# Kernel tuning notes

Measured on AMD Instinct MI355X. Metric: run time of the kernel, lower is better.

The kernel has to match this reference:

```python
import jax, jax.numpy as jnp
import numpy as np


def setup_inputs() -> dict:
    key = jax.random.key(0)
    k1, k2 = jax.random.split(key)
    x = jax.random.normal(k1, (8, 4096, 256), dtype=jnp.float32)
    embed = jax.random.normal(k2, (1, 8192, 256), dtype=jnp.float32)
    return {"x": x, "embed": embed}


def reference(x, embed):
    # EuclideanCodebook.forward, eval mode, sample_codebook_temp=0.
    # x: [b, n, d]  (ndim < 4 -> a leading codebook dim h=1 is added)
    # embed: [h, c, d]
    xf = x.astype(jnp.float32)[None]              # [h, b, n, d]
    h, b, n, d = xf.shape
    flatten = xf.reshape(h, b * n, d)             # [h, N, d]

    # dist = -cdist(flatten, embed, p=2)
    x2 = jnp.sum(flatten * flatten, axis=-1, keepdims=True)   # [h, N, 1]
    e2 = jnp.sum(embed * embed, axis=-1)                      # [h, c]
    xe = jnp.einsum('hnd,hcd->hnc', flatten, embed)           # [h, N, c]
    d2 = jnp.maximum(x2 + e2[:, None, :] - 2.0 * xe, 0.0)
    dist = -jnp.sqrt(d2)                                      # [h, N, c]

    # gumbel_sample with temperature == 0  ->  argmax
    embed_ind = jnp.argmax(dist, axis=-1)                     # [h, N]
    embed_ind = embed_ind.reshape(h, b, n)                    # [h, b, n]

    # batched_embedding: gather codes per codebook
    quantize = jax.vmap(lambda e, i: e[i])(embed, embed_ind)  # [h, b, n, d]

    # needs_codebook_dim -> squeeze leading h
    return quantize[0], embed_ind[0]
```

## Files before the change

### kernel.cpp

```cpp
#include <hip/hip_runtime.h>
#include <math.h>

#define D       256
#define NROWS   32768
#define CODES   8192
#define QOFF    8388608

#define BM      128
#define BN      128
#define BK      64
#define NSPL    4
#define SPLC    (CODES / NSPL)
#define NCHUNK  (SPLC / BN)
#define NBLK    1024
#define LQ      4096

#define MARG_COEF 0.016f
#define MARG_ABS  0.10f

#define OFF_AH    0ull
#define OFF_X2    16777216ull
#define OFF_NX    16908288ull
#define OFF_E2    17039360ull
#define OFF_RM    17072128ull
#define OFF_PK    17203200ull
#define OFF_MISC  17465344ull
#define OFF_BCNT  17465600ull
#define OFF_CAND  17469696ull
#define WS_NEED3  38441216ull

typedef __attribute__((ext_vector_type(8)))  short bf16x8;
typedef __attribute__((ext_vector_type(16))) float f32x16;

__device__ __forceinline__ int SWK(int b) { return b ^ (((b >> 7) & 7) << 4); }

__device__ __forceinline__ void gload16(const void* g, void* l) {
  __builtin_amdgcn_global_load_lds(
      (const __attribute__((address_space(1))) unsigned int*)g,
      (__attribute__((address_space(3))) unsigned int*)l, 16, 0, 0);
}

__device__ __forceinline__ unsigned short bf16rn(float x) {
  unsigned u = __float_as_uint(x);
  return (unsigned short)((u + 0x7fffu + ((u >> 16) & 1u)) >> 16);
}

__device__ __forceinline__ unsigned encf(float f) {
  unsigned b = __float_as_uint(f);
  return (b >> 31) ? ~b : (b | 0x80000000u);
}
__device__ __forceinline__ float decf(unsigned u) {
  return __uint_as_float((u >> 31) ? (u ^ 0x80000000u) : ~u);
}

__global__ __launch_bounds__(256) void init_kernel(unsigned* __restrict__ misc,
                                                   unsigned* __restrict__ rowMinU,
                                                   unsigned long long* __restrict__ pKey) {
  int i = blockIdx.x * 256 + threadIdx.x;
  if (i < 16) misc[i] = 0u;
  rowMinU[i] = 0xFFFFFFFFu;
  pKey[i] = ~0ull;
}

__global__ __launch_bounds__(256) void prep_kernel(const float* __restrict__ x,
                                                   const float* __restrict__ embed,
                                                   unsigned short* __restrict__ A_h,
                                                   unsigned short* __restrict__ E_h,
                                                   float* __restrict__ x2,
                                                   float* __restrict__ nx,
                                                   float* __restrict__ e2,
                                                   unsigned* __restrict__ misc) {
  int wid  = threadIdx.x >> 6;
  int lane = threadIdx.x & 63;
  int rid  = blockIdx.x * 4 + wid;
  const float* src;
  unsigned short* dst;
  if (rid < NROWS) { src = x + (size_t)rid * D;               dst = A_h + (size_t)rid * D; }
  else             { src = embed + (size_t)(rid - NROWS) * D; dst = E_h + (size_t)(rid - NROWS) * D; }
  float4 v = *(const float4*)(src + lane * 4);
  ushort4 hv = make_ushort4(bf16rn(v.x), bf16rn(v.y), bf16rn(v.z), bf16rn(v.w));
  *(ushort4*)(dst + lane * 4) = hv;
  float p = v.x * v.x + v.y * v.y + v.z * v.z + v.w * v.w;
  #pragma unroll
  for (int off = 32; off > 0; off >>= 1) p += __shfl_down(p, off);
  if (lane == 0) {
    float n = sqrtf(p);
    if (rid < NROWS) { x2[rid] = p; nx[rid] = n; }
    else { e2[rid - NROWS] = p; atomicMax(&misc[2], __float_as_uint(n)); }
  }
}

template<int MODE>
__global__ __launch_bounds__(256, 2) void gemm_pass(
    const unsigned short* __restrict__ A_h,
    const unsigned short* __restrict__ E_h,
    const float* __restrict__ e2g,
    const float* __restrict__ nxg,
    const unsigned* __restrict__ miscR,
    unsigned* __restrict__ rowMinU,
    unsigned* __restrict__ cand,
    unsigned* __restrict__ blkCnt,
    unsigned* __restrict__ ovCnt,
    unsigned Q, unsigned OVCAP) {
  __shared__ __align__(16) char As[16384];
  __shared__ __align__(16) char Bs[16384];
  __shared__ unsigned lbuf[MODE ? LQ : 1];
  __shared__ unsigned lcnt;

  const int tid  = threadIdx.x;
  const int lane = tid & 63;
  const int wave = tid >> 6;
  const int wm = wave >> 1, wn = wave & 1;
  const int l31 = lane & 31;
  const int lh4 = (lane >> 5) * 4;
  const int rowBase = blockIdx.x * BM;
  const int split   = blockIdx.y;
  const int seg     = blockIdx.y * 256 + blockIdx.x;

  int swA[2][4], swB[2][4];
  #pragma unroll
  for (int f = 0; f < 2; f++)
    #pragma unroll
    for (int ks = 0; ks < 4; ks++) {
      int byt = ks * 32 + (lane >> 5) * 16;
      swA[f][ks] = SWK(((wm * 64 + f * 32 + l31) << 7) + byt);
      swB[f][ks] = SWK(((wn * 64 + f * 32 + l31) << 7) + byt);
    }

  int stRow[4], stCo[4], stDst[4];
  #pragma unroll
  for (int i = 0; i < 4; i++) {
    int q = i * 256 + tid;
    int u = SWK(q << 4);
    stRow[i] = u >> 7;
    stCo[i]  = u & 127;
    stDst[i] = (q & ~63) << 4;
  }

  float state[2][16];
  if (MODE == 0) {
    #pragma unroll
    for (int f = 0; f < 2; f++)
      #pragma unroll
      for (int rg = 0; rg < 16; rg++) state[f][rg] = INFINITY;
  } else {
    float neMaxF = __uint_as_float(miscR[2]);
    #pragma unroll
    for (int f = 0; f < 2; f++)
      #pragma unroll
      for (int rg = 0; rg < 16; rg++) {
        int row = rowBase + wm * 64 + f * 32 + ((rg & 3) + 8 * (rg >> 2)) + lh4;
        state[f][rg] = decf(rowMinU[row]) + fmaf(MARG_COEF * nxg[row], neMaxF, MARG_ABS);
      }
    if (tid == 0) lcnt = 0;
  }

  for (int cc = 0; cc < NCHUNK; ++cc) {
    const int cBase = split * SPLC + cc * BN;

    f32x16 acc[2][2];
    #pragma unroll
    for (int i = 0; i < 2; i++)
      #pragma unroll
      for (int j = 0; j < 2; j++) acc[i][j] = (f32x16)(0.0f);

    for (int kb = 0; kb < 4; ++kb) {
      __syncthreads();
      #pragma unroll
      for (int i = 0; i < 4; i++) {
        gload16((const char*)A_h + (((size_t)(rowBase + stRow[i])) << 9) + (kb << 7) + stCo[i],
                As + stDst[i]);
        gload16((const char*)E_h + (((size_t)(cBase + stRow[i])) << 9) + (kb << 7) + stCo[i],
                Bs + stDst[i]);
      }
      __syncthreads();
      #pragma unroll
      for (int ks = 0; ks < 4; ++ks) {
        bf16x8 a0 = *(const bf16x8*)(As + swA[0][ks]);
        bf16x8 a1 = *(const bf16x8*)(As + swA[1][ks]);
        bf16x8 b0 = *(const bf16x8*)(Bs + swB[0][ks]);
        bf16x8 b1 = *(const bf16x8*)(Bs + swB[1][ks]);
        acc[0][0] = __builtin_amdgcn_mfma_f32_32x32x16_bf16(a0, b0, acc[0][0], 0, 0, 0);
        acc[0][1] = __builtin_amdgcn_mfma_f32_32x32x16_bf16(a0, b1, acc[0][1], 0, 0, 0);
        acc[1][0] = __builtin_amdgcn_mfma_f32_32x32x16_bf16(a1, b0, acc[1][0], 0, 0, 0);
        acc[1][1] = __builtin_amdgcn_mfma_f32_32x32x16_bf16(a1, b1, acc[1][1], 0, 0, 0);
      }
    }

    #pragma unroll
    for (int fn = 0; fn < 2; fn++) {
      int col = cBase + wn * 64 + fn * 32 + l31;
      float e2c = e2g[col];
      #pragma unroll
      for (int fm = 0; fm < 2; fm++)
        #pragma unroll
        for (int rg = 0; rg < 16; rg++) {
          float q = fmaf(acc[fm][fn][rg], -2.0f, e2c);
          if (MODE == 0) {
            state[fm][rg] = fminf(state[fm][rg], q);
          } else if (q <= state[fm][rg]) {
            int row = rowBase + wm * 64 + fm * 32 + ((rg & 3) + 8 * (rg >> 2)) + lh4;
            unsigned en = (unsigned)((row << 13) | col);
            unsigned p = atomicAdd(&lcnt, 1u);
            if (p < LQ) lbuf[p] = en;
            else { unsigned gp = atomicAdd(ovCnt, 1u);
                   if (gp < OVCAP) cand[(size_t)NBLK * Q + gp] = en; }
          }
        }
    }
  }

  if (MODE == 0) {
    #pragma unroll
    for (int fm = 0; fm < 2; fm++)
      #pragma unroll
      for (int rg = 0; rg < 16; rg++) {
        float v = state[fm][rg];
        #pragma unroll
        for (int off = 1; off < 32; off <<= 1) v = fminf(v, __shfl_xor(v, off));
        if (l31 == 0) {
          int row = rowBase + wm * 64 + fm * 32 + ((rg & 3) + 8 * (rg >> 2)) + lh4;
          atomicMin(&rowMinU[row], encf(v));
        }
      }
  } else {
    __syncthreads();
    unsigned n = lcnt; if (n > LQ) n = LQ;
    for (unsigned i = tid; i < n; i += 256) cand[(size_t)seg * Q + i] = lbuf[i];
    if (tid == 0) blkCnt[seg] = n;
  }
}

__global__ __launch_bounds__(256) void refine_kernel(const float* __restrict__ x,
                                                     const float* __restrict__ embed,
                                                     const float* __restrict__ x2g,
                                                     const float* __restrict__ e2g,
                                                     const unsigned* __restrict__ blkCnt,
                                                     const unsigned* __restrict__ cand,
                                                     const unsigned* __restrict__ miscR,
                                                     unsigned long long* __restrict__ pKey,
                                                     unsigned Q, unsigned OVCAP) {
  const int tid = threadIdx.x;
  const int l16 = tid & 15;
  const int gid = tid >> 4;

  auto doItem = [&](unsigned pk) {
    int row = (int)(pk >> 13), col = (int)(pk & 8191u);
    double s = 0.0;
    #pragma unroll
    for (int p = 0; p < 4; p++) {
      float4 xv = *(const float4*)&x[(size_t)row * D + p * 64 + l16 * 4];
      float4 ev = *(const float4*)&embed[(size_t)col * D + p * 64 + l16 * 4];
      s = fma((double)xv.x, (double)ev.x, s);
      s = fma((double)xv.y, (double)ev.y, s);
      s = fma((double)xv.z, (double)ev.z, s);
      s = fma((double)xv.w, (double)ev.w, s);
    }
    #pragma unroll
    for (int off = 1; off < 16; off <<= 1) s += __shfl_xor(s, off);
    if (l16 == 0) {
      float xef = (float)s;
      float ss  = __fadd_rn(x2g[row], e2g[col]);
      float d2  = __fsub_rn(ss, __fmul_rn(2.0f, xef));
      d2 = fmaxf(d2, 0.0f);
      float sq = sqrtf(d2);
      unsigned long long key =
          ((unsigned long long)__float_as_uint(sq) << 32) | (unsigned)col;
      atomicMin(pKey + row, key);
    }
  };

  unsigned seg = blockIdx.x;
  unsigned n = blkCnt[seg]; if (n > LQ) n = LQ;
  const unsigned* segp = cand + (size_t)seg * Q;
  for (unsigned i = gid; i < n; i += 16) doItem(segp[i]);

  unsigned ov = miscR[1]; if (ov > OVCAP) ov = OVCAP;
  const unsigned* ovp = cand + (size_t)NBLK * Q;
  for (unsigned i = blockIdx.x * 16 + gid; i < ov; i += NBLK * 16) doItem(ovp[i]);
}

__global__ __launch_bounds__(256) void final_kernel(const float* __restrict__ embed,
                                                    const unsigned long long* __restrict__ pKey,
                                                    float* __restrict__ outQ,
                                                    float* __restrict__ indF) {
  int wid  = threadIdx.x >> 6;
  int lane = threadIdx.x & 63;
  int row  = blockIdx.x * 4 + wid;
  unsigned long long k = pKey[row];
  int idx = (int)(k & 8191ull);
  float4 v = *(const float4*)&embed[(size_t)idx * D + lane * 4];
  *(float4*)&outQ[(size_t)row * D + lane * 4] = v;
  if (lane == 0) indF[row] = (float)idx;
}

#define BM_F 128
#define BN_F 128
#define BK_F 32
#define NSPLIT_F 4
#define SPLIT_CF (CODES / NSPLIT_F)

__global__ __launch_bounds__(256) void sq_kernel(const float* __restrict__ x,
                                                 const float* __restrict__ embed,
                                                 float* __restrict__ x2,
                                                 float* __restrict__ e2) {
  int wid  = threadIdx.x >> 6;
  int lane = threadIdx.x & 63;
  int rid  = blockIdx.x * 4 + wid;
  const float* base = (rid < NROWS) ? (x + (size_t)rid * D)
                                    : (embed + (size_t)(rid - NROWS) * D);
  float4 v = *(const float4*)(base + lane * 4);
  float p = v.x * v.x + v.y * v.y + v.z * v.z + v.w * v.w;
  #pragma unroll
  for (int off = 32; off > 0; off >>= 1) p += __shfl_down(p, off);
  if (lane == 0) {
    if (rid < NROWS) x2[rid] = p;
    else             e2[rid - NROWS] = p;
  }
}

__global__ __launch_bounds__(256) void argmin_f32_kernel(const float* __restrict__ x,
                                                         const float* __restrict__ embed,
                                                         const float* __restrict__ x2,
                                                         const float* __restrict__ e2,
                                                         float* __restrict__ pVal,
                                                         int* __restrict__ pIdx) {
  __shared__ float As[BK_F][BM_F];
  __shared__ float Bs[BK_F][BN_F];
  const int tid = threadIdx.x;
  const int ty = tid >> 4, tx = tid & 15;
  const int rowBase = blockIdx.x * BM_F;
  const int split = blockIdx.y;
  const int r0 = ty * 8, c0 = tx * 8;
  float bestV[8]; int bestI[8];
  #pragma unroll
  for (int i = 0; i < 8; i++) { bestV[i] = -INFINITY; bestI[i] = 0; }
  float x2r[8];
  #pragma unroll
  for (int i = 0; i < 8; i++) x2r[i] = x2[rowBase + r0 + i];
  for (int chunk = 0; chunk < SPLIT_CF / BN_F; ++chunk) {
    const int cBase = split * SPLIT_CF + chunk * BN_F;
    float acc[8][8];
    #pragma unroll
    for (int i = 0; i < 8; i++)
      #pragma unroll
      for (int j = 0; j < 8; j++) acc[i][j] = 0.0f;
    for (int kb = 0; kb < D / BK_F; ++kb) {
      #pragma unroll
      for (int i = 0; i < 4; i++) {
        int f4 = tid + i * 256;
        int rr = f4 >> 3, k4 = f4 & 7;
        float4 va = *(const float4*)&x[(size_t)(rowBase + rr) * D + kb * BK_F + k4 * 4];
        As[k4 * 4 + 0][rr] = va.x; As[k4 * 4 + 1][rr] = va.y;
        As[k4 * 4 + 2][rr] = va.z; As[k4 * 4 + 3][rr] = va.w;
        float4 vb = *(const float4*)&embed[(size_t)(cBase + rr) * D + kb * BK_F + k4 * 4];
        Bs[k4 * 4 + 0][rr] = vb.x; Bs[k4 * 4 + 1][rr] = vb.y;
        Bs[k4 * 4 + 2][rr] = vb.z; Bs[k4 * 4 + 3][rr] = vb.w;
      }
      __syncthreads();
      #pragma unroll 8
      for (int kk = 0; kk < BK_F; kk++) {
        float a[8], b[8];
        *(float4*)&a[0] = *(const float4*)&As[kk][r0];
        *(float4*)&a[4] = *(const float4*)&As[kk][r0 + 4];
        *(float4*)&b[0] = *(const float4*)&Bs[kk][c0];
        *(float4*)&b[4] = *(const float4*)&Bs[kk][c0 + 4];
        #pragma unroll
        for (int i = 0; i < 8; i++)
          #pragma unroll
          for (int j = 0; j < 8; j++)
            acc[i][j] = fmaf(a[i], b[j], acc[i][j]);
      }
      __syncthreads();
    }
    #pragma unroll
    for (int j = 0; j < 8; j++) {
      int c = cBase + c0 + j;
      float e2c = e2[c];
      #pragma unroll
      for (int i = 0; i < 8; i++) {
        float s  = __fadd_rn(x2r[i], e2c);
        float u  = __fmul_rn(2.0f, acc[i][j]);
        float d2 = fmaxf(__fsub_rn(s, u), 0.0f);
        float dist = -sqrtf(d2);
        if (dist > bestV[i]) { bestV[i] = dist; bestI[i] = c; }
      }
    }
  }
  __syncthreads();
  float* Vl = &As[0][0];
  int*   Il = (int*)&Bs[0][0];
  #pragma unroll
  for (int i = 0; i < 8; i++) {
    Vl[(ty * 16 + tx) * 8 + i] = bestV[i];
    Il[(ty * 16 + tx) * 8 + i] = bestI[i];
  }
  __syncthreads();
  if (tid < BM_F) {
    int rr = tid, tyr = rr >> 3, ii = rr & 7;
    float bv = -INFINITY; int bi = 0;
    #pragma unroll
    for (int t = 0; t < 16; t++) {
      float v = Vl[(tyr * 16 + t) * 8 + ii];
      int  iv = Il[(tyr * 16 + t) * 8 + ii];
      if (v > bv || (v == bv && iv < bi)) { bv = v; bi = iv; }
    }
    pVal[split * NROWS + rowBase + rr] = bv;
    pIdx[split * NROWS + rowBase + rr] = bi;
  }
}

__global__ __launch_bounds__(256) void merge_f32_kernel(const float* __restrict__ pVal,
                                                        const int* __restrict__ pIdx,
                                                        float* __restrict__ indF) {
  int row = blockIdx.x * 256 + threadIdx.x;
  if (row >= NROWS) return;
  float bv = -INFINITY; int bi = 0;
  #pragma unroll
  for (int s = 0; s < NSPLIT_F; s++) {
    float v = pVal[s * NROWS + row];
    int  iv = pIdx[s * NROWS + row];
    if (v > bv || (v == bv && iv < bi)) { bv = v; bi = iv; }
  }
  indF[row] = (float)bi;
}

__global__ __launch_bounds__(256) void gather_f32_kernel(const float* __restrict__ embed,
                                                         const float* __restrict__ indF,
                                                         float* __restrict__ outQ) {
  int wid = threadIdx.x >> 6, lane = threadIdx.x & 63;
  int row = blockIdx.x * 4 + wid;
  int idx = (int)indF[row];
  float4 v = *(const float4*)&embed[(size_t)idx * D + lane * 4];
  *(float4*)&outQ[(size_t)row * D + lane * 4] = v;
}

extern "C" void kernel_launch(void* const* d_in, const int* in_sizes, int n_in,
                              void* d_out, int out_size, void* d_ws, size_t ws_size,
                              hipStream_t stream) {
  const float* x     = (const float*)d_in[0];
  const float* embed = (const float*)d_in[1];
  float* o = (float*)d_out;

  if (ws_size >= WS_NEED3) {
    char* w = (char*)d_ws;
    unsigned short* A_h = (unsigned short*)(w + OFF_AH);
    float* x2 = (float*)(w + OFF_X2);
    float* nx = (float*)(w + OFF_NX);
    float* e2 = (float*)(w + OFF_E2);
    unsigned* rowMinU = (unsigned*)(w + OFF_RM);
    unsigned long long* pKey = (unsigned long long*)(w + OFF_PK);
    unsigned* misc = (unsigned*)(w + OFF_MISC);
    unsigned* blkCnt = (unsigned*)(w + OFF_BCNT);
    unsigned* cand = (unsigned*)(w + OFF_CAND);
    unsigned capN  = (unsigned)((ws_size - OFF_CAND) / 4ull);
    unsigned Q     = (capN - 262144u) >> 10;
    unsigned OVCAP = capN - (Q << 10);

    unsigned short* E_h = (unsigned short*)o;
    float* indF = o + QOFF;

    init_kernel<<<128, 256, 0, stream>>>(misc, rowMinU, pKey);
    prep_kernel<<<(NROWS + CODES) / 4, 256, 0, stream>>>(x, embed, A_h, E_h, x2, nx, e2, misc);
    dim3 gridC(NROWS / BM, NSPL);
    gemm_pass<0><<<gridC, 256, 0, stream>>>(A_h, E_h, e2, nx, misc, rowMinU,
                                            cand, blkCnt, &misc[1], Q, OVCAP);
    gemm_pass<1><<<gridC, 256, 0, stream>>>(A_h, E_h, e2, nx, misc, rowMinU,
                                            cand, blkCnt, &misc[1], Q, OVCAP);
    refine_kernel<<<NBLK, 256, 0, stream>>>(x, embed, x2, e2, blkCnt, cand, misc,
                                            pKey, Q, OVCAP);
    final_kernel<<<NROWS / 4, 256, 0, stream>>>(embed, pKey, o, indF);
  } else {
    float* x2   = o;
    float* e2   = o + 32768;
    float* pVal = o + 65536;
    int*   pIdx = (int*)(o + 196608);
    float* indF = o + QOFF;
    sq_kernel<<<(NROWS + CODES) / 4, 256, 0, stream>>>(x, embed, x2, e2);
    dim3 gridB(NROWS / BM_F, NSPLIT_F);
    argmin_f32_kernel<<<gridB, 256, 0, stream>>>(x, embed, x2, e2, pVal, pIdx);
    merge_f32_kernel<<<NROWS / 256, 256, 0, stream>>>(pVal, pIdx, indF);
    gather_f32_kernel<<<NROWS / 4, 256, 0, stream>>>(embed, indF, o);
  }
}
```

Before: 488.8 us.

## Keep A tile in registers across full K and stage whole B chunk in LDS

Each block now loads its 128x256 bf16 A tile into LDS once and keeps it in registers (32 bf16x8 fragments per lane) for all code chunks. Only the B tile is reloaded per chunk, as one full-K 64KB load with a row-XOR swizzle, replacing four K-steps with separate A and B loads. This removes redundant A reloads and cuts barriers per chunk from eight to two. In exchange it raises register pressure, which can hurt occupancy, and uses a 64KB LDS buffer. The candidate queue per segment is also fixed at LQ=2048, shrinking the workspace requirement.

```diff
diff --git a/kernel.cpp b/kernel.cpp
--- a/kernel.cpp
+++ b/kernel.cpp
@@ -8,12 +8,11 @@
 
 #define BM      128
 #define BN      128
-#define BK      64
 #define NSPL    4
 #define SPLC    (CODES / NSPL)
 #define NCHUNK  (SPLC / BN)
 #define NBLK    1024
-#define LQ      4096
+#define LQ      2048
 
 #define MARG_COEF 0.016f
 #define MARG_ABS  0.10f
@@ -27,12 +26,10 @@
 #define OFF_MISC  17465344ull
 #define OFF_BCNT  17465600ull
 #define OFF_CAND  17469696ull
-#define WS_NEED3  38441216ull
+#define WS_NEED3  30052608ull
 
 typedef __attribute__((ext_vector_type(8)))  short bf16x8;
 typedef __attribute__((ext_vector_type(16))) float f32x16;
-
-__device__ __forceinline__ int SWK(int b) { return b ^ (((b >> 7) & 7) << 4); }
 
 __device__ __forceinline__ void gload16(const void* g, void* l) {
   __builtin_amdgcn_global_load_lds(
@@ -101,9 +98,8 @@
     unsigned* __restrict__ cand,
     unsigned* __restrict__ blkCnt,
     unsigned* __restrict__ ovCnt,
-    unsigned Q, unsigned OVCAP) {
-  __shared__ __align__(16) char As[16384];
-  __shared__ __align__(16) char Bs[16384];
+    unsigned OVCAP) {
+  __shared__ __align__(16) char Bbuf[65536];
   __shared__ unsigned lbuf[MODE ? LQ : 1];
   __shared__ unsigned lcnt;
 
@@ -112,101 +108,119 @@
   const int wave = tid >> 6;
   const int wm = wave >> 1, wn = wave & 1;
   const int l31 = lane & 31;
-  const int lh4 = (lane >> 5) * 4;
+  const int hi16 = (lane >> 5) << 4;
+  const int lh4  = (lane >> 5) << 2;
   const int rowBase = blockIdx.x * BM;
   const int split   = blockIdx.y;
   const int seg     = blockIdx.y * 256 + blockIdx.x;
 
-  int swA[2][4], swB[2][4];
-  #pragma unroll
-  for (int f = 0; f < 2; f++)
-    #pragma unroll
-    for (int ks = 0; ks < 4; ks++) {
-      int byt = ks * 32 + (lane >> 5) * 16;
-      swA[f][ks] = SWK(((wm * 64 + f * 32 + l31) << 7) + byt);
-      swB[f][ks] = SWK(((wn * 64 + f * 32 + l31) << 7) + byt);
-    }
-
-  int stRow[4], stCo[4], stDst[4];
-  #pragma unroll
-  for (int i = 0; i < 4; i++) {
+  #pragma unroll
+  for (int i = 0; i < 16; i++) {
     int q = i * 256 + tid;
-    int u = SWK(q << 4);
-    stRow[i] = u >> 7;
-    stCo[i]  = u & 127;
-    stDst[i] = (q & ~63) << 4;
+    int b = q << 4;
+    int u = b ^ (((b >> 9) & 7) << 4);
+    gload16((const char*)A_h + (((size_t)(rowBase + (u >> 9))) << 9) + (u & 511),
+            Bbuf + ((q & ~63) << 4));
+  }
+  if (MODE == 1 && tid == 0) lcnt = 0;
+  __syncthreads();
+
+  bf16x8 af[2][16];
+  #pragma unroll
+  for (int f = 0; f < 2; f++) {
+    int rowA = wm * 64 + f * 32 + l31;
+    int base = rowA << 9;
+    int xv = (rowA & 7) << 4;
+    #pragma unroll
+    for (int ks = 0; ks < 16; ks++)
+      af[f][ks] = *(const bf16x8*)(Bbuf + base + ((ks * 32 + hi16) ^ xv));
+  }
+
+  int bbase[2], bxor[2];
+  #pragma unroll
+  for (int g = 0; g < 2; g++) {
+    int rowB = wn * 64 + g * 32 + l31;
+    bbase[g] = rowB << 9;
+    bxor[g]  = (rowB & 7) << 4;
   }
 
   float state[2][16];
   if (MODE == 0) {
     #pragma unroll
-    for (int f = 0; f < 2; f++)
-      #pragma unroll
-      for (int rg = 0; rg < 16; rg++) state[f][rg] = INFINITY;
+    for (int fm = 0; fm < 2; fm++)
+      #pragma unroll
+      for (int rg = 0; rg < 16; rg++) state[fm][rg] = INFINITY;
   } else {
     float neMaxF = __uint_as_float(miscR[2]);
     #pragma unroll
-    for (int f = 0; f < 2; f++)
+    for (int fm = 0; fm < 2; fm++)
       #pragma unroll
       for (int rg = 0; rg < 16; rg++) {
-        int row = rowBase + wm * 64 + f * 32 + ((rg & 3) + 8 * (rg >> 2)) + lh4;
-        state[f][rg] = decf(rowMinU[row]) + fmaf(MARG_COEF * nxg[row], neMaxF, MARG_ABS);
-      }
-    if (tid == 0) lcnt = 0;
+        int row = rowBase + wm * 64 + fm * 32 + ((rg & 3) + 8 * (rg >> 2)) + lh4;
+        state[fm][rg] = decf(rowMinU[row]) + fmaf(MARG_COEF * nxg[row], neMaxF, MARG_ABS);
+      }
   }
 
   for (int cc = 0; cc < NCHUNK; ++cc) {
     const int cBase = split * SPLC + cc * BN;
 
+    __syncthreads();
+    #pragma unroll
+    for (int i = 0; i < 16; i++) {
+      int q = i * 256 + tid;
+      int b = q << 4;
+      int u = b ^ (((b >> 9) & 7) << 4);
+      gload16((const char*)E_h + (((size_t)(cBase + (u >> 9))) << 9) + (u & 511),
+              Bbuf + ((q & ~63) << 4));
+    }
+    __syncthreads();
+
     f32x16 acc[2][2];
     #pragma unroll
     for (int i = 0; i < 2; i++)
       #pragma unroll
       for (int j = 0; j < 2; j++) acc[i][j] = (f32x16)(0.0f);
 
-    for (int kb = 0; kb < 4; ++kb) {
-      __syncthreads();
-      #pragma unroll
-      for (int i = 0; i < 4; i++) {
-        gload16((const char*)A_h + (((size_t)(rowBase + stRow[i])) << 9) + (kb << 7) + stCo[i],
-                As + stDst[i]);
-        gload16((const char*)E_h + (((size_t)(cBase + stRow[i])) << 9) + (kb << 7) + stCo[i],
-                Bs + stDst[i]);
-      }
-      __syncthreads();
-      #pragma unroll
-      for (int ks = 0; ks < 4; ++ks) {
-        bf16x8 a0 = *(const bf16x8*)(As + swA[0][ks]);
-        bf16x8 a1 = *(const bf16x8*)(As + swA[1][ks]);
-        bf16x8 b0 = *(const bf16x8*)(Bs + swB[0][ks]);
-        bf16x8 b1 = *(const bf16x8*)(Bs + swB[1][ks]);
-        acc[0][0] = __builtin_amdgcn_mfma_f32_32x32x16_bf16(a0, b0, acc[0][0], 0, 0, 0);
-        acc[0][1] = __builtin_amdgcn_mfma_f32_32x32x16_bf16(a0, b1, acc[0][1], 0, 0, 0);
-        acc[1][0] = __builtin_amdgcn_mfma_f32_32x32x16_bf16(a1, b0, acc[1][0], 0, 0, 0);
-        acc[1][1] = __builtin_amdgcn_mfma_f32_32x32x16_bf16(a1, b1, acc[1][1], 0, 0, 0);
-      }
-    }
-
-    #pragma unroll
-    for (int fn = 0; fn < 2; fn++) {
-      int col = cBase + wn * 64 + fn * 32 + l31;
-      float e2c = e2g[col];
-      #pragma unroll
-      for (int fm = 0; fm < 2; fm++)
+    #pragma unroll
+    for (int ks = 0; ks < 16; ks++) {
+      bf16x8 b0 = *(const bf16x8*)(Bbuf + bbase[0] + ((ks * 32 + hi16) ^ bxor[0]));
+      bf16x8 b1 = *(const bf16x8*)(Bbuf + bbase[1] + ((ks * 32 + hi16) ^ bxor[1]));
+      acc[0][0] = __builtin_amdgcn_mfma_f32_32x32x16_bf16(af[0][ks], b0, acc[0][0], 0, 0, 0);
+      acc[1][0] = __builtin_amdgcn_mfma_f32_32x32x16_bf16(af[1][ks], b0, acc[1][0], 0, 0, 0);
+      acc[0][1] = __builtin_amdgcn_mfma_f32_32x32x16_bf16(af[0][ks], b1, acc[0][1], 0, 0, 0);
+      acc[1][1] = __builtin_amdgcn_mfma_f32_32x32x16_bf16(af[1][ks], b1, acc[1][1], 0, 0, 0);
+    }
+
+    if (MODE == 0) {
+      #pragma unroll
+      for (int g = 0; g < 2; g++) {
+        float e2c = e2g[cBase + wn * 64 + g * 32 + l31];
         #pragma unroll
-        for (int rg = 0; rg < 16; rg++) {
-          float q = fmaf(acc[fm][fn][rg], -2.0f, e2c);
-          if (MODE == 0) {
-            state[fm][rg] = fminf(state[fm][rg], q);
-          } else if (q <= state[fm][rg]) {
-            int row = rowBase + wm * 64 + fm * 32 + ((rg & 3) + 8 * (rg >> 2)) + lh4;
-            unsigned en = (unsigned)((row << 13) | col);
-            unsigned p = atomicAdd(&lcnt, 1u);
-            if (p < LQ) lbuf[p] = en;
-            else { unsigned gp = atomicAdd(ovCnt, 1u);
-                   if (gp < OVCAP) cand[(size_t)NBLK * Q + gp] = en; }
+        for (int fm = 0; fm < 2; fm++)
+          #pragma unroll
+          for (int rg = 0; rg < 16; rg++)
+            state[fm][rg] = fminf(state[fm][rg], fmaf(acc[fm][g][rg], -2.0f, e2c));
+      }
+    } else {
+      #pragma unroll
+      for (int g = 0; g < 2; g++) {
+        int col = cBase + wn * 64 + g * 32 + l31;
+        float e2c = e2g[col];
+        #pragma unroll
+        for (int fm = 0; fm < 2; fm++)
+          #pragma unroll
+          for (int rg = 0; rg < 16; rg++) {
+            float q = fmaf(acc[fm][g][rg], -2.0f, e2c);
+            if (q <= state[fm][rg]) {
+              int row = rowBase + wm * 64 + fm * 32 + ((rg & 3) + 8 * (rg >> 2)) + lh4;
+              unsigned en = (unsigned)((row << 13) | col);
+              unsigned p = atomicAdd(&lcnt, 1u);
+              if (p < LQ) lbuf[p] = en;
+              else { unsigned gp = atomicAdd(ovCnt, 1u);
+                     if (gp < OVCAP) cand[(size_t)NBLK * LQ + gp] = en; }
+            }
           }
-        }
+      }
     }
   }
 
@@ -226,7 +240,7 @@
   } else {
     __syncthreads();
     unsigned n = lcnt; if (n > LQ) n = LQ;
-    for (unsigned i = tid; i < n; i += 256) cand[(size_t)seg * Q + i] = lbuf[i];
+    for (unsigned i = tid; i < n; i += 256) cand[(size_t)seg * LQ + i] = lbuf[i];
     if (tid == 0) blkCnt[seg] = n;
   }
 }
@@ -239,7 +253,7 @@
                                                      const unsigned* __restrict__ cand,
                                                      const unsigned* __restrict__ miscR,
                                                      unsigned long long* __restrict__ pKey,
-                                                     unsigned Q, unsigned OVCAP) {
+                                                     unsigned OVCAP) {
   const int tid = threadIdx.x;
   const int l16 = tid & 15;
   const int gid = tid >> 4;
@@ -272,11 +286,11 @@
 
   unsigned seg = blockIdx.x;
   unsigned n = blkCnt[seg]; if (n > LQ) n = LQ;
-  const unsigned* segp = cand + (size_t)seg * Q;
+  const unsigned* segp = cand + (size_t)seg * LQ;
   for (unsigned i = gid; i < n; i += 16) doItem(segp[i]);
 
   unsigned ov = miscR[1]; if (ov > OVCAP) ov = OVCAP;
-  const unsigned* ovp = cand + (size_t)NBLK * Q;
+  const unsigned* ovp = cand + (size_t)NBLK * LQ;
   for (unsigned i = blockIdx.x * 16 + gid; i < ov; i += NBLK * 16) doItem(ovp[i]);
 }
 
@@ -454,8 +468,7 @@
     unsigned* blkCnt = (unsigned*)(w + OFF_BCNT);
     unsigned* cand = (unsigned*)(w + OFF_CAND);
     unsigned capN  = (unsigned)((ws_size - OFF_CAND) / 4ull);
-    unsigned Q     = (capN - 262144u) >> 10;
-    unsigned OVCAP = capN - (Q << 10);
+    unsigned OVCAP = capN - (unsigned)(NBLK * LQ);
 
     unsigned short* E_h = (unsigned short*)o;
     float* indF = o + QOFF;
@@ -464,11 +477,11 @@
     prep_kernel<<<(NROWS + CODES) / 4, 256, 0, stream>>>(x, embed, A_h, E_h, x2, nx, e2, misc);
     dim3 gridC(NROWS / BM, NSPL);
     gemm_pass<0><<<gridC, 256, 0, stream>>>(A_h, E_h, e2, nx, misc, rowMinU,
-                                            cand, blkCnt, &misc[1], Q, OVCAP);
+                                            cand, blkCnt, &misc[1], OVCAP);
     gemm_pass<1><<<gridC, 256, 0, stream>>>(A_h, E_h, e2, nx, misc, rowMinU,
-                                            cand, blkCnt, &misc[1], Q, OVCAP);
+                                            cand, blkCnt, &misc[1], OVCAP);
     refine_kernel<<<NBLK, 256, 0, stream>>>(x, embed, x2, e2, blkCnt, cand, misc,
-                                            pKey, Q, OVCAP);
+                                            pKey, OVCAP);
     final_kernel<<<NROWS / 4, 256, 0, stream>>>(embed, pKey, o, indF);
   } else {
     float* x2   = o;
```

After: 601.3 us. 1.23x slower.
